# Kernel tuning notes

Measured on AMD Instinct MI355X. Metric: run time of the kernel, lower is better.

The kernel has to match this reference:

```python
import jax, jax.numpy as jnp
import numpy as np
import math

B, T, EMB = 2, 2048, 2048
HQ = HKV = 16
HD = EMB // HQ  # 128
MAX_SEQ = 2048


def _rope(x, cos, sin):
    # x: [b, t, h, d]; pairs are consecutive (view_as_complex on reshape(..., -1, 2))
    b, t, h, d = x.shape
    xp = x.astype(jnp.float32).reshape(b, t, h, d // 2, 2)
    xr, xi = xp[..., 0], xp[..., 1]
    c = cos[None, :, None, :]  # [1, t, 1, d/2]
    s = sin[None, :, None, :]
    or_ = xr * c - xi * s
    oi_ = xr * s + xi * c
    out = jnp.stack([or_, oi_], axis=-1).reshape(b, t, h, d)
    return out.astype(x.dtype)


def setup_inputs() -> dict:
    key = jax.random.key(0)
    ks = jax.random.split(key, 6)
    x = jax.random.normal(ks[0], (B, T, EMB), dtype=jnp.float32)
    # torch Linear weights: [out_features, in_features], y = x @ W.T
    sc = 1.0 / math.sqrt(EMB)
    wq = jax.random.normal(ks[1], (EMB, EMB), dtype=jnp.float32) * sc
    wk = jax.random.normal(ks[2], (EMB, EMB), dtype=jnp.float32) * sc
    wv = jax.random.normal(ks[3], (EMB, EMB), dtype=jnp.float32) * sc
    wo = jax.random.normal(ks[4], (EMB, EMB), dtype=jnp.float32) * sc
    # RoPE frequencies (llama-style), head_dim/2 angles per position
    inv_freq = 1.0 / (10000.0 ** (np.arange(0, HD, 2, dtype=np.float32) / HD))
    angles = np.arange(T, dtype=np.float32)[:, None] * inv_freq[None, :]  # [T, HD/2]
    freqs_cos = jnp.asarray(np.cos(angles))
    freqs_sin = jnp.asarray(np.sin(angles))
    k_cache = jnp.zeros((B, MAX_SEQ, HKV, HD), dtype=jnp.float32)
    v_cache = jnp.zeros((B, MAX_SEQ, HKV, HD), dtype=jnp.float32)
    return {"x": x, "wq": wq, "wk": wk, "wv": wv, "wo": wo,
            "k_cache": k_cache, "v_cache": v_cache,
            "freqs_cos": freqs_cos, "freqs_sin": freqs_sin, "start_pos": 0}


def reference(x, wq, wk, wv, wo, k_cache, v_cache, freqs_cos, freqs_sin, start_pos):
    b, t, c = x.shape
    xq = (x @ wq.T).reshape(b, t, HQ, HD)
    xk = (x @ wk.T).reshape(b, t, HKV, HD)
    xv = (x @ wv.T).reshape(b, t, HKV, HD)
    xq = _rope(xq, freqs_cos, freqs_sin)
    xk = _rope(xk, freqs_cos, freqs_sin)
    # KV-cache update at start_pos, then read prefix [0, start_pos+t)
    k_cache = jax.lax.dynamic_update_slice(k_cache, xk, (0, start_pos, 0, 0))
    v_cache = jax.lax.dynamic_update_slice(v_cache, xv, (0, start_pos, 0, 0))
    keys = k_cache[:, :start_pos + t]    # [b, s, hkv, d]
    values = v_cache[:, :start_pos + t]
    # n_rep = HQ // HKV = 1 -> repeat_kv is identity
    q = xq.transpose(0, 2, 1, 3)         # [b, h, t, d]
    k = keys.transpose(0, 2, 1, 3)       # [b, h, s, d]
    v = values.transpose(0, 2, 1, 3)
    scores = jnp.einsum('bhtd,bhsd->bhts', q, k) / math.sqrt(HD)
    scores = jax.nn.softmax(scores.astype(jnp.float32), axis=-1).astype(q.dtype)
    out = jnp.einsum('bhts,bhsd->bhtd', scores, v)
    out = out.transpose(0, 2, 1, 3).reshape(b, t, -1)
    return out @ wo.T
```

## Files before the change

kernel.cpp:

```cpp
#include <hip/hip_runtime.h>
#include <cstdint>

using u16 = unsigned short;
using short8 = __attribute__((ext_vector_type(8))) short;
using floatx4 = __attribute__((ext_vector_type(4))) float;

__device__ __forceinline__ u16 f2b(float f) {
    unsigned u = __float_as_uint(f);
    u = (u + 0x7fffu + ((u >> 16) & 1u)) >> 16;
    return (u16)u;
}
__device__ __forceinline__ u16 f2b_fast(float f) {
    return (u16)((__float_as_uint(f) + 0x8000u) >> 16);
}
__device__ __forceinline__ float b2f(unsigned v) {
    return __uint_as_float(v << 16);
}
__device__ __forceinline__ float fast_exp2(float f) {
#if __has_builtin(__builtin_amdgcn_exp2f)
    return __builtin_amdgcn_exp2f(f);
#else
    return exp2f(f);
#endif
}
__device__ __forceinline__ void gl_lds16(const u16* g, u16* l) {
    __builtin_amdgcn_global_load_lds(
        (const __attribute__((address_space(1))) void*)(const void*)g,
        (__attribute__((address_space(3))) void*)(void*)l, 16, 0, 0);
}

__global__ void cvt_kernel(const float* __restrict__ in, u16* __restrict__ out, int n) {
    int i = (blockIdx.x * 256 + threadIdx.x) * 4;
    if (i >= n) return;
    float4 v = *(const float4*)&in[i];
    uint2 o;
    o.x = (unsigned)f2b(v.x) | ((unsigned)f2b(v.y) << 16);
    o.y = (unsigned)f2b(v.z) | ((unsigned)f2b(v.w) << 16);
    *(uint2*)&out[i] = o;
}

template <int OUT_F32>
__global__ void gemm_bt(const u16* __restrict__ A, const u16* __restrict__ B,
                        void* __restrict__ Cp, int M, int N, int K) {
    __shared__ u16 As[128 * 32];
    __shared__ u16 Bs[128 * 32];
    const int tid = threadIdx.x;
    const int lane = tid & 63, w = tid >> 6;
    const int wm = w & 1, wn = w >> 1;
    const int m0 = blockIdx.y * 128, n0 = blockIdx.x * 128;
    const int r = lane & 15, q = lane >> 4;

    floatx4 acc[4][4] = {};

    for (int k0 = 0; k0 < K; k0 += 32) {
        __syncthreads();
#pragma unroll
        for (int i = 0; i < 2; i++) {
            int c = i * 256 + tid;
            int row = c >> 2, c8 = (c & 3) * 8;
            gl_lds16(A + (size_t)(m0 + row) * K + k0 + c8, As + c * 8);
            gl_lds16(B + (size_t)(n0 + row) * K + k0 + c8, Bs + c * 8);
        }
        __syncthreads();
        short8 af[4], bf[4];
#pragma unroll
        for (int mi = 0; mi < 4; mi++)
            af[mi] = *(const short8*)&As[(wm * 64 + mi * 16 + r) * 32 + q * 8];
#pragma unroll
        for (int ni = 0; ni < 4; ni++)
            bf[ni] = *(const short8*)&Bs[(wn * 64 + ni * 16 + r) * 32 + q * 8];
#pragma unroll
        for (int mi = 0; mi < 4; mi++)
#pragma unroll
            for (int ni = 0; ni < 4; ni++)
                acc[mi][ni] = __builtin_amdgcn_mfma_f32_16x16x32_bf16(af[mi], bf[ni], acc[mi][ni], 0, 0, 0);
    }
#pragma unroll
    for (int mi = 0; mi < 4; mi++)
#pragma unroll
        for (int ni = 0; ni < 4; ni++)
#pragma unroll
            for (int rr = 0; rr < 4; rr++) {
                int row = m0 + wm * 64 + mi * 16 + q * 4 + rr;
                int col = n0 + wn * 64 + ni * 16 + r;
                if (OUT_F32)
                    ((float*)Cp)[(size_t)row * N + col] = acc[mi][ni][rr];
                else
                    ((u16*)Cp)[(size_t)row * N + col] = f2b(acc[mi][ni][rr]);
            }
}

__global__ void rope_kernel(u16* __restrict__ xqkv, const float* __restrict__ fc,
                            const float* __restrict__ fs) {
    int tid = blockIdx.x * 256 + threadIdx.x;
    int d2 = tid & 63;
    int h = (tid >> 6) & 15;
    int t = (tid >> 10) & 2047;
    int b = tid >> 21;
    float c = fc[t * 64 + d2], s = fs[t * 64 + d2];
    int base = (b * 2048 + t) * 6144 + h * 128 + d2 * 2;
    unsigned uq = *(unsigned*)&xqkv[base];
    float xr = b2f(uq & 0xffffu), xi = b2f(uq >> 16);
    *(unsigned*)&xqkv[base] =
        (unsigned)f2b(xr * c - xi * s) | ((unsigned)f2b(xr * s + xi * c) << 16);
    unsigned uk = *(unsigned*)&xqkv[base + 2048];
    xr = b2f(uk & 0xffffu); xi = b2f(uk >> 16);
    *(unsigned*)&xqkv[base + 2048] =
        (unsigned)f2b(xr * c - xi * s) | ((unsigned)f2b(xr * s + xi * c) << 16);
}

__global__ void vtrans_kernel(const u16* __restrict__ xqkv, u16* __restrict__ vt) {
    __shared__ u16 Ts[64][72];
    int bh = blockIdx.z, d0 = blockIdx.y * 64, t0 = blockIdx.x * 64;
    int b = bh >> 4, h = bh & 15;
#pragma unroll
    for (int i = 0; i < 2; i++) {
        int c = i * 256 + threadIdx.x;
        int tr = c >> 3, c8 = (c & 7) * 8;
        short8 v = *(const short8*)&xqkv[(size_t)(b * 2048 + t0 + tr) * 6144 + 4096 + h * 128 + d0 + c8];
#pragma unroll
        for (int j = 0; j < 8; j++) Ts[tr][c8 + j] = ((u16)v[j]);
    }
    __syncthreads();
#pragma unroll
    for (int i = 0; i < 2; i++) {
        int c = i * 256 + threadIdx.x;
        int dr = c >> 3, t8 = (c & 7) * 8;
        short8 v;
#pragma unroll
        for (int j = 0; j < 8; j++) v[j] = (short)Ts[t8 + j][dr];
        *(short8*)&vt[((size_t)(bh * 128 + d0 + dr)) * 2048 + t0 + t8] = v;
    }
}

__global__ __launch_bounds__(256, 2) void flash_kernel(const u16* __restrict__ xqkv,
                                                       const u16* __restrict__ vt,
                                                       u16* __restrict__ ao) {
    __shared__ u16 smem[25600];
    u16* Ks = smem;
    u16* Vs = smem + 8192;
    const int tid = threadIdx.x;
    const int lane = tid & 63, w = tid >> 6;
    const int qg = lane >> 4, r16 = lane & 15;
    u16* QPw = smem + 16384 + w * 2304;
    const int bh = blockIdx.y, b = bh >> 4, h = bh & 15;
    const int t0 = blockIdx.x * 128 + w * 32;
    const float sl2e = 0.08838834764831845f * 1.4426950408889634f;

    short8 qreg[2][4];
#pragma unroll
    for (int tf = 0; tf < 2; tf++)
#pragma unroll
        for (int kc = 0; kc < 4; kc++) {
            short8 qv = *(const short8*)&xqkv[(size_t)(b * 2048 + t0 + tf * 16 + r16) * 6144 +
                                              h * 128 + kc * 32 + qg * 8];
#pragma unroll
            for (int j = 0; j < 8; j++)
                qv[j] = (short)f2b(b2f((u16)qv[j]) * sl2e);
            qreg[tf][kc] = qv;
        }

    floatx4 oacc[2][8] = {};
    float lsum[2][4] = {};

    for (int s0 = 0; s0 < 2048; s0 += 64) {
        __syncthreads();
#pragma unroll
        for (int i = 0; i < 4; i++) {
            int c = i * 256 + tid;
            int kc = c >> 8, cc = c & 255, sr = cc >> 2, e8 = (cc & 3) * 8;
            gl_lds16(xqkv + (size_t)(b * 2048 + s0 + sr) * 6144 + 2048 + h * 128 + kc * 32 + e8,
                     Ks + c * 8);
        }
#pragma unroll
        for (int i = 0; i < 4; i++) {
            int c = i * 256 + tid;
            int sc = c >> 9, cc = c & 511, d = cc >> 2, e8 = (cc & 3) * 8;
            gl_lds16(vt + (size_t)(bh * 128 + d) * 2048 + s0 + sc * 32 + e8, Vs + c * 8);
        }
        __syncthreads();

        floatx4 sacc[2][4] = {};
#pragma unroll
        for (int kc = 0; kc < 4; kc++)
#pragma unroll
            for (int ni = 0; ni < 4; ni++) {
                short8 bfr = *(const short8*)&Ks[kc * 2048 + (ni * 16 + r16) * 32 + qg * 8];
                sacc[0][ni] = __builtin_amdgcn_mfma_f32_16x16x32_bf16(qreg[0][kc], bfr, sacc[0][ni], 0, 0, 0);
                sacc[1][ni] = __builtin_amdgcn_mfma_f32_16x16x32_bf16(qreg[1][kc], bfr, sacc[1][ni], 0, 0, 0);
            }

#pragma unroll
        for (int tf = 0; tf < 2; tf++)
#pragma unroll
            for (int ni = 0; ni < 4; ni++)
#pragma unroll
                for (int r = 0; r < 4; r++) {
                    float p = fast_exp2(sacc[tf][ni][r]);
                    lsum[tf][r] += p;
                    QPw[(tf * 16 + qg * 4 + r) * 72 + ni * 16 + r16] = f2b_fast(p);
                }

#pragma unroll
        for (int sc = 0; sc < 2; sc++) {
            short8 p0 = *(const short8*)&QPw[(r16) * 72 + sc * 32 + qg * 8];
            short8 p1 = *(const short8*)&QPw[(16 + r16) * 72 + sc * 32 + qg * 8];
#pragma unroll
            for (int dt = 0; dt < 8; dt++) {
                short8 a = *(const short8*)&Vs[sc * 4096 + (dt * 16 + r16) * 32 + qg * 8];
                oacc[0][dt] = __builtin_amdgcn_mfma_f32_16x16x32_bf16(a, p0, oacc[0][dt], 0, 0, 0);
                oacc[1][dt] = __builtin_amdgcn_mfma_f32_16x16x32_bf16(a, p1, oacc[1][dt], 0, 0, 0);
            }
        }
    }

#pragma unroll
    for (int mm = 1; mm <= 8; mm <<= 1)
#pragma unroll
        for (int tf = 0; tf < 2; tf++)
#pragma unroll
            for (int r = 0; r < 4; r++) lsum[tf][r] += __shfl_xor(lsum[tf][r], mm);

    int src = (r16 >> 2) << 4;
#pragma unroll
    for (int tf = 0; tf < 2; tf++) {
        float l0 = __shfl(lsum[tf][0], src), l1 = __shfl(lsum[tf][1], src);
        float l2 = __shfl(lsum[tf][2], src), l3 = __shfl(lsum[tf][3], src);
        float lsel = (r16 & 2) ? ((r16 & 1) ? l3 : l2) : ((r16 & 1) ? l1 : l0);
        float inv = 1.0f / lsel;
#pragma unroll
        for (int dt = 0; dt < 8; dt++)
#pragma unroll
            for (int r = 0; r < 4; r++)
                QPw[r16 * 136 + dt * 16 + qg * 4 + r] = f2b(oacc[tf][dt][r] * inv);
#pragma unroll
        for (int i = 0; i < 4; i++) {
            int c = i * 64 + lane;
            int rowt = c >> 4, c8 = (c & 15) * 8;
            short8 v = *(const short8*)&QPw[rowt * 136 + c8];
            *(short8*)&ao[(size_t)(b * 2048 + t0 + tf * 16 + rowt) * 2048 + h * 128 + c8] = v;
        }
    }
}

extern "C" void kernel_launch(void* const* d_in, const int* in_sizes, int n_in,
                              void* d_out, int out_size, void* d_ws, size_t ws_size,
                              hipStream_t stream) {
    const float* x = (const float*)d_in[0];
    const float* wq = (const float*)d_in[1];
    const float* wk = (const float*)d_in[2];
    const float* wv = (const float*)d_in[3];
    const float* wo = (const float*)d_in[4];
    const float* fcos = (const float*)d_in[7];
    const float* fsin = (const float*)d_in[8];

    char* ws = (char*)d_ws;
    u16* xb    = (u16*)(ws);
    u16* wqkvb = (u16*)(ws + 16777216);
    u16* wob   = (u16*)(ws + 41943040);
    u16* xqkv  = (u16*)(ws + 50331648);
    u16* vt    = (u16*)(ws + 100663296);
    u16* ao    = (u16*)(ws + 117440512);

    cvt_kernel<<<8192, 256, 0, stream>>>(x, xb, 8388608);
    cvt_kernel<<<4096, 256, 0, stream>>>(wq, wqkvb, 4194304);
    cvt_kernel<<<4096, 256, 0, stream>>>(wk, wqkvb + 4194304, 4194304);
    cvt_kernel<<<4096, 256, 0, stream>>>(wv, wqkvb + 8388608, 4194304);
    cvt_kernel<<<4096, 256, 0, stream>>>(wo, wob, 4194304);

    gemm_bt<0><<<dim3(48, 32), 256, 0, stream>>>(xb, wqkvb, xqkv, 4096, 6144, 2048);
    rope_kernel<<<16384, 256, 0, stream>>>(xqkv, fcos, fsin);
    vtrans_kernel<<<dim3(32, 2, 32), 256, 0, stream>>>(xqkv, vt);
    flash_kernel<<<dim3(16, 32), 256, 0, stream>>>(xqkv, vt, ao);
    gemm_bt<1><<<dim3(16, 32), 256, 0, stream>>>(ao, wob, (float*)d_out, 4096, 2048, 2048);
}
```

Baseline: 456.7 us.

## Swizzle LDS tiles to avoid bank conflicts and merge prep kernel launches

```diff
diff --git a/kernel.cpp b/kernel.cpp
--- a/kernel.cpp
+++ b/kernel.cpp
@@ -29,14 +29,24 @@
         (__attribute__((address_space(3))) void*)(void*)l, 16, 0, 0);
 }
 
-__global__ void cvt_kernel(const float* __restrict__ in, u16* __restrict__ out, int n) {
-    int i = (blockIdx.x * 256 + threadIdx.x) * 4;
-    if (i >= n) return;
-    float4 v = *(const float4*)&in[i];
+__global__ void cvt5_kernel(const float* __restrict__ x, const float* __restrict__ wq,
+                            const float* __restrict__ wk, const float* __restrict__ wv,
+                            const float* __restrict__ wo, u16* __restrict__ xb,
+                            u16* __restrict__ wqkvb, u16* __restrict__ wob) {
+    int i = blockIdx.x * 256 + threadIdx.x;
+    const float* src;
+    u16* dst;
+    int off;
+    if (i < 2097152)      { src = x;  dst = xb;             off = i; }
+    else if (i < 3145728) { src = wq; dst = wqkvb;          off = i - 2097152; }
+    else if (i < 4194304) { src = wk; dst = wqkvb + 4194304; off = i - 3145728; }
+    else if (i < 5242880) { src = wv; dst = wqkvb + 8388608; off = i - 4194304; }
+    else                  { src = wo; dst = wob;            off = i - 5242880; }
+    float4 v = ((const float4*)src)[off];
     uint2 o;
     o.x = (unsigned)f2b(v.x) | ((unsigned)f2b(v.y) << 16);
     o.y = (unsigned)f2b(v.z) | ((unsigned)f2b(v.w) << 16);
-    *(uint2*)&out[i] = o;
+    *(uint2*)&dst[off * 4] = o;
 }
 
 template <int OUT_F32>
@@ -49,6 +59,7 @@
     const int wm = w & 1, wn = w >> 1;
     const int m0 = blockIdx.y * 128, n0 = blockIdx.x * 128;
     const int r = lane & 15, q = lane >> 4;
+    const int sw = (q ^ ((r >> 1) & 3)) * 8;
 
     floatx4 acc[4][4] = {};
 
@@ -57,18 +68,19 @@
 #pragma unroll
         for (int i = 0; i < 2; i++) {
             int c = i * 256 + tid;
-            int row = c >> 2, c8 = (c & 3) * 8;
-            gl_lds16(A + (size_t)(m0 + row) * K + k0 + c8, As + c * 8);
-            gl_lds16(B + (size_t)(n0 + row) * K + k0 + c8, Bs + c * 8);
+            int row = c >> 2, slot = c & 3;
+            int sch = (slot ^ ((row >> 1) & 3)) * 8;
+            gl_lds16(A + (size_t)(m0 + row) * K + k0 + sch, As + c * 8);
+            gl_lds16(B + (size_t)(n0 + row) * K + k0 + sch, Bs + c * 8);
         }
         __syncthreads();
         short8 af[4], bf[4];
 #pragma unroll
         for (int mi = 0; mi < 4; mi++)
-            af[mi] = *(const short8*)&As[(wm * 64 + mi * 16 + r) * 32 + q * 8];
+            af[mi] = *(const short8*)&As[(wm * 64 + mi * 16 + r) * 32 + sw];
 #pragma unroll
         for (int ni = 0; ni < 4; ni++)
-            bf[ni] = *(const short8*)&Bs[(wn * 64 + ni * 16 + r) * 32 + q * 8];
+            bf[ni] = *(const short8*)&Bs[(wn * 64 + ni * 16 + r) * 32 + sw];
 #pragma unroll
         for (int mi = 0; mi < 4; mi++)
 #pragma unroll
@@ -90,46 +102,47 @@
             }
 }
 
-__global__ void rope_kernel(u16* __restrict__ xqkv, const float* __restrict__ fc,
-                            const float* __restrict__ fs) {
-    int tid = blockIdx.x * 256 + threadIdx.x;
-    int d2 = tid & 63;
-    int h = (tid >> 6) & 15;
-    int t = (tid >> 10) & 2047;
-    int b = tid >> 21;
-    float c = fc[t * 64 + d2], s = fs[t * 64 + d2];
-    int base = (b * 2048 + t) * 6144 + h * 128 + d2 * 2;
-    unsigned uq = *(unsigned*)&xqkv[base];
-    float xr = b2f(uq & 0xffffu), xi = b2f(uq >> 16);
-    *(unsigned*)&xqkv[base] =
-        (unsigned)f2b(xr * c - xi * s) | ((unsigned)f2b(xr * s + xi * c) << 16);
-    unsigned uk = *(unsigned*)&xqkv[base + 2048];
-    xr = b2f(uk & 0xffffu); xi = b2f(uk >> 16);
-    *(unsigned*)&xqkv[base + 2048] =
-        (unsigned)f2b(xr * c - xi * s) | ((unsigned)f2b(xr * s + xi * c) << 16);
-}
-
-__global__ void vtrans_kernel(const u16* __restrict__ xqkv, u16* __restrict__ vt) {
-    __shared__ u16 Ts[64][72];
-    int bh = blockIdx.z, d0 = blockIdx.y * 64, t0 = blockIdx.x * 64;
-    int b = bh >> 4, h = bh & 15;
-#pragma unroll
-    for (int i = 0; i < 2; i++) {
-        int c = i * 256 + threadIdx.x;
-        int tr = c >> 3, c8 = (c & 7) * 8;
-        short8 v = *(const short8*)&xqkv[(size_t)(b * 2048 + t0 + tr) * 6144 + 4096 + h * 128 + d0 + c8];
-#pragma unroll
-        for (int j = 0; j < 8; j++) Ts[tr][c8 + j] = ((u16)v[j]);
-    }
-    __syncthreads();
-#pragma unroll
-    for (int i = 0; i < 2; i++) {
-        int c = i * 256 + threadIdx.x;
-        int dr = c >> 3, t8 = (c & 7) * 8;
-        short8 v;
-#pragma unroll
-        for (int j = 0; j < 8; j++) v[j] = (short)Ts[t8 + j][dr];
-        *(short8*)&vt[((size_t)(bh * 128 + d0 + dr)) * 2048 + t0 + t8] = v;
+__global__ void prep_kernel(u16* __restrict__ xqkv, const float* __restrict__ fc,
+                            const float* __restrict__ fs, u16* __restrict__ vt) {
+    if (blockIdx.x < 16384) {
+        int tid = blockIdx.x * 256 + threadIdx.x;
+        int d2 = tid & 63;
+        int h = (tid >> 6) & 15;
+        int t = (tid >> 10) & 2047;
+        int b = tid >> 21;
+        float c = fc[t * 64 + d2], s = fs[t * 64 + d2];
+        int base = (b * 2048 + t) * 6144 + h * 128 + d2 * 2;
+        unsigned uq = *(unsigned*)&xqkv[base];
+        float xr = b2f(uq & 0xffffu), xi = b2f(uq >> 16);
+        *(unsigned*)&xqkv[base] =
+            (unsigned)f2b(xr * c - xi * s) | ((unsigned)f2b(xr * s + xi * c) << 16);
+        unsigned uk = *(unsigned*)&xqkv[base + 2048];
+        xr = b2f(uk & 0xffffu); xi = b2f(uk >> 16);
+        *(unsigned*)&xqkv[base + 2048] =
+            (unsigned)f2b(xr * c - xi * s) | ((unsigned)f2b(xr * s + xi * c) << 16);
+    } else {
+        __shared__ u16 Ts[64][72];
+        int vb = blockIdx.x - 16384;
+        int t0 = (vb & 31) * 64, d0 = ((vb >> 5) & 1) * 64, bh = vb >> 6;
+        int b = bh >> 4, h = bh & 15;
+#pragma unroll
+        for (int i = 0; i < 2; i++) {
+            int c = i * 256 + threadIdx.x;
+            int tr = c >> 3, c8 = (c & 7) * 8;
+            short8 v = *(const short8*)&xqkv[(size_t)(b * 2048 + t0 + tr) * 6144 + 4096 + h * 128 + d0 + c8];
+#pragma unroll
+            for (int j = 0; j < 8; j++) Ts[tr][c8 + j] = ((u16)v[j]);
+        }
+        __syncthreads();
+#pragma unroll
+        for (int i = 0; i < 2; i++) {
+            int c = i * 256 + threadIdx.x;
+            int dr = c >> 3, t8 = (c & 7) * 8;
+            short8 v;
+#pragma unroll
+            for (int j = 0; j < 8; j++) v[j] = (short)Ts[t8 + j][dr];
+            *(short8*)&vt[((size_t)(bh * 128 + d0 + dr)) * 2048 + t0 + t8] = v;
+        }
     }
 }
 
@@ -142,6 +155,7 @@
     const int tid = threadIdx.x;
     const int lane = tid & 63, w = tid >> 6;
     const int qg = lane >> 4, r16 = lane & 15;
+    const int swz = (qg ^ ((r16 >> 1) & 3)) * 8;
     u16* QPw = smem + 16384 + w * 2304;
     const int bh = blockIdx.y, b = bh >> 4, h = bh & 15;
     const int t0 = blockIdx.x * 128 + w * 32;
@@ -168,15 +182,17 @@
 #pragma unroll
         for (int i = 0; i < 4; i++) {
             int c = i * 256 + tid;
-            int kc = c >> 8, cc = c & 255, sr = cc >> 2, e8 = (cc & 3) * 8;
-            gl_lds16(xqkv + (size_t)(b * 2048 + s0 + sr) * 6144 + 2048 + h * 128 + kc * 32 + e8,
+            int kc = c >> 8, cc = c & 255, sr = cc >> 2, slot = cc & 3;
+            int sch = (slot ^ ((sr >> 1) & 3)) * 8;
+            gl_lds16(xqkv + (size_t)(b * 2048 + s0 + sr) * 6144 + 2048 + h * 128 + kc * 32 + sch,
                      Ks + c * 8);
         }
 #pragma unroll
         for (int i = 0; i < 4; i++) {
             int c = i * 256 + tid;
-            int sc = c >> 9, cc = c & 511, d = cc >> 2, e8 = (cc & 3) * 8;
-            gl_lds16(vt + (size_t)(bh * 128 + d) * 2048 + s0 + sc * 32 + e8, Vs + c * 8);
+            int sc = c >> 9, cc = c & 511, d = cc >> 2, slot = cc & 3;
+            int sch = (slot ^ ((d >> 1) & 3)) * 8;
+            gl_lds16(vt + (size_t)(bh * 128 + d) * 2048 + s0 + sc * 32 + sch, Vs + c * 8);
         }
         __syncthreads();
 
@@ -185,7 +201,7 @@
         for (int kc = 0; kc < 4; kc++)
 #pragma unroll
             for (int ni = 0; ni < 4; ni++) {
-                short8 bfr = *(const short8*)&Ks[kc * 2048 + (ni * 16 + r16) * 32 + qg * 8];
+                short8 bfr = *(const short8*)&Ks[kc * 2048 + (ni * 16 + r16) * 32 + swz];
                 sacc[0][ni] = __builtin_amdgcn_mfma_f32_16x16x32_bf16(qreg[0][kc], bfr, sacc[0][ni], 0, 0, 0);
                 sacc[1][ni] = __builtin_amdgcn_mfma_f32_16x16x32_bf16(qreg[1][kc], bfr, sacc[1][ni], 0, 0, 0);
             }
@@ -207,7 +223,7 @@
             short8 p1 = *(const short8*)&QPw[(16 + r16) * 72 + sc * 32 + qg * 8];
 #pragma unroll
             for (int dt = 0; dt < 8; dt++) {
-                short8 a = *(const short8*)&Vs[sc * 4096 + (dt * 16 + r16) * 32 + qg * 8];
+                short8 a = *(const short8*)&Vs[sc * 4096 + (dt * 16 + r16) * 32 + swz];
                 oacc[0][dt] = __builtin_amdgcn_mfma_f32_16x16x32_bf16(a, p0, oacc[0][dt], 0, 0, 0);
                 oacc[1][dt] = __builtin_amdgcn_mfma_f32_16x16x32_bf16(a, p1, oacc[1][dt], 0, 0, 0);
             }
@@ -262,15 +278,9 @@
     u16* vt    = (u16*)(ws + 100663296);
     u16* ao    = (u16*)(ws + 117440512);
 
-    cvt_kernel<<<8192, 256, 0, stream>>>(x, xb, 8388608);
-    cvt_kernel<<<4096, 256, 0, stream>>>(wq, wqkvb, 4194304);
-    cvt_kernel<<<4096, 256, 0, stream>>>(wk, wqkvb + 4194304, 4194304);
-    cvt_kernel<<<4096, 256, 0, stream>>>(wv, wqkvb + 8388608, 4194304);
-    cvt_kernel<<<4096, 256, 0, stream>>>(wo, wob, 4194304);
-
+    cvt5_kernel<<<24576, 256, 0, stream>>>(x, wq, wk, wv, wo, xb, wqkvb, wob);
     gemm_bt<0><<<dim3(48, 32), 256, 0, stream>>>(xb, wqkvb, xqkv, 4096, 6144, 2048);
-    rope_kernel<<<16384, 256, 0, stream>>>(xqkv, fcos, fsin);
-    vtrans_kernel<<<dim3(32, 2, 32), 256, 0, stream>>>(xqkv, vt);
+    prep_kernel<<<18432, 256, 0, stream>>>(xqkv, fcos, fsin, vt);
     flash_kernel<<<dim3(16, 32), 256, 0, stream>>>(xqkv, vt, ao);
     gemm_bt<1><<<dim3(16, 32), 256, 0, stream>>>(ao, wob, (float*)d_out, 4096, 2048, 2048);
 }
```

Measured after the change: 441.8 us. 3.3% less time.
